# Performance work log

Hardware: AMD Instinct MI355X
Metric: run time of the kernel (lower is better)

## Reference

```python
import jax, jax.numpy as jnp
import numpy as np

B, TK, H = 32, 8192, 256

def setup_inputs() -> dict:
    key = jax.random.key(0)
    ks = jax.random.split(key, 10)
    s = 0.02
    return {
        "s_t_hat": jax.random.normal(ks[0], (B, 2 * H), dtype=jnp.float32),
        "encoder_outputs": jax.random.normal(ks[1], (B, TK, H), dtype=jnp.float32),
        "enc_padding_mask": jnp.ones((B, TK), dtype=jnp.float32),
        "coverage": jax.random.uniform(ks[2], (B, TK), dtype=jnp.float32),
        "attn_dist_node_to_token": jax.random.uniform(ks[3], (B, TK), dtype=jnp.float32),
        "We": jax.random.normal(ks[4], (H, H), dtype=jnp.float32) * s,   # encode_proj weight
        "Wd": jax.random.normal(ks[5], (H, 2 * H), dtype=jnp.float32) * s,  # decode_proj weight
        "bd": jax.random.normal(ks[6], (H,), dtype=jnp.float32) * s,     # decode_proj bias
        "wc": jax.random.normal(ks[7], (H,), dtype=jnp.float32) * s,     # W_c weight (Linear(1,H))
        "v": jax.random.normal(ks[8], (H,), dtype=jnp.float32) * s,      # v weight (Linear(H,1))
    }

def reference(s_t_hat, encoder_outputs, enc_padding_mask, coverage,
              attn_dist_node_to_token, We, Wd, bd, wc, v):
    # encoder projection: [b,t,h] @ We^T -> [b,t,h]
    enc_feat = jnp.einsum('bth,gh->btg', encoder_outputs, We)
    # decoder projection: [b,2h] @ Wd^T + bd -> [b,h]
    dec_fea = s_t_hat @ Wd.T + bd
    # coverage feature: outer product coverage[b,t] x wc[h]
    att_features = enc_feat + dec_fea[:, None, :] + coverage[..., None] * wc
    e = jnp.tanh(att_features)
    scores = jnp.einsum('bth,h->bt', e, v)  # [b, t_k]
    attn_ = jax.nn.softmax(scores, axis=1) * enc_padding_mask
    attn = attn_ / jnp.sum(attn_, axis=1, keepdims=True)
    c_t = jnp.einsum('bt,bth->bh', attn, encoder_outputs)  # context
    new_cov = jnp.clip(coverage + attn, 0.0, 1.0)
    return (c_t, attn, new_cov)
```

## Files before the change

### kernel.cpp

```cpp
#include <hip/hip_runtime.h>

#define B_  32
#define TK_ 8192
#define H_  256
#define MT  64

typedef __bf16 bf16_t;
typedef __bf16 bf16x4 __attribute__((ext_vector_type(4)));
typedef __bf16 bf16x8 __attribute__((ext_vector_type(8)));
typedef float  floatx4 __attribute__((ext_vector_type(4)));

__device__ __forceinline__ float tanh_fast(float x) {
    float e = __builtin_amdgcn_exp2f(x * 2.885390081777927f);
    return 1.0f - 2.0f * __builtin_amdgcn_rcpf(e + 1.0f);
}

__global__ void prep_kernel(const float* __restrict__ s_t_hat,
                            const float* __restrict__ We,
                            const float* __restrict__ Wd,
                            const float* __restrict__ bd,
                            bf16_t* __restrict__ We_bf,
                            float* __restrict__ dec_ws,
                            float* __restrict__ ctx_ws,
                            float* __restrict__ D_ws) {
    int tid = threadIdx.x, blk = blockIdx.x;
    int gid = blk * 256 + tid;
    We_bf[gid] = (bf16_t)We[gid];

    if (blk < 32) {
        ctx_ws[gid] = 0.f;
        if (gid < 32) D_ws[gid] = 0.f;
    }
    if (blk >= 32 && blk < 160) {
        int idx  = (blk - 32) * 256 + tid;
        int pair = idx >> 2, q = idx & 3;
        int b = pair >> 8, i = pair & 255;
        const float4* sp = (const float4*)(s_t_hat + b * 2 * H_ + q * 128);
        const float4* wp = (const float4*)(Wd + (size_t)i * 2 * H_ + q * 128);
        float sum = 0.f;
        #pragma unroll 8
        for (int ii = 0; ii < 32; ++ii) {
            float4 a = sp[ii], w = wp[ii];
            sum += a.x * w.x + a.y * w.y + a.z * w.z + a.w * w.w;
        }
        sum += __shfl_xor(sum, 1, 64);
        sum += __shfl_xor(sum, 2, 64);
        if (q == 0) dec_ws[pair] = sum + bd[i];
    }
}

__global__ __launch_bounds__(256, 3) void attn_main(
    const float* __restrict__ enc,
    const float* __restrict__ mask,
    const float* __restrict__ cov,
    const float* __restrict__ wc,
    const float* __restrict__ v,
    const bf16_t* __restrict__ We_bf,
    const float* __restrict__ dec_ws,
    float* __restrict__ ctx_ws,
    float* __restrict__ D_ws,
    float* __restrict__ attn_out) {

    __shared__ __align__(16) bf16_t As[MT * 264];
    __shared__ float dec_s[256], wc_s[256], v_s[256];
    __shared__ float cov_s[64], mask_s[64], wexp[64];
    __shared__ float sp[4][64];
    __shared__ float ctxp[4][256];

    const int tid  = threadIdx.x;
    const int b    = blockIdx.y;
    const int t0   = blockIdx.x * MT;
    const int lane = tid & 63, w = tid >> 6;
    const int l15  = lane & 15, l4 = lane >> 4;

    dec_s[tid] = dec_ws[b * 256 + tid];
    wc_s[tid]  = wc[tid];
    v_s[tid]   = v[tid];
    if (tid < 64)       cov_s[tid]       = cov[(size_t)b * TK_ + t0 + tid];
    else if (tid < 128) mask_s[tid - 64] = mask[(size_t)b * TK_ + t0 + tid - 64];

    const float* encb = enc + ((size_t)b * TK_ + t0) * H_;
    #pragma unroll
    for (int it = 0; it < 16; ++it) {
        int row = it * 4 + w;
        int h   = lane * 4;
        float4 f = *(const float4*)(encb + (size_t)row * H_ + h);
        bf16x4 p;
        p[0] = (bf16_t)f.x; p[1] = (bf16_t)f.y; p[2] = (bf16_t)f.z; p[3] = (bf16_t)f.w;
        *(bf16x4*)(&As[row * 264 + h]) = p;
    }
    __syncthreads();

    floatx4 acc[4][4];
    #pragma unroll
    for (int mi = 0; mi < 4; ++mi)
        #pragma unroll
        for (int ni = 0; ni < 4; ++ni)
            acc[mi][ni] = (floatx4){0.f, 0.f, 0.f, 0.f};

    const int wbase = w * 64;
    #pragma unroll
    for (int ks = 0; ks < 8; ++ks) {
        int k = ks * 32 + l4 * 8;
        bf16x8 a[4], bq[4];
        #pragma unroll
        for (int mi = 0; mi < 4; ++mi)
            a[mi] = *(const bf16x8*)(&As[(mi * 16 + l15) * 264 + k]);
        #pragma unroll
        for (int ni = 0; ni < 4; ++ni)
            bq[ni] = *(const bf16x8*)(We_bf + (size_t)(wbase + ni * 16 + l15) * 256 + k);
        #pragma unroll
        for (int mi = 0; mi < 4; ++mi)
            #pragma unroll
            for (int ni = 0; ni < 4; ++ni)
                acc[mi][ni] = __builtin_amdgcn_mfma_f32_16x16x32_bf16(
                    a[mi], bq[ni], acc[mi][ni], 0, 0, 0);
    }

    float decv[4], wcv[4], vv[4];
    #pragma unroll
    for (int ni = 0; ni < 4; ++ni) {
        int g = wbase + ni * 16 + l15;
        decv[ni] = dec_s[g]; wcv[ni] = wc_s[g]; vv[ni] = v_s[g];
    }
    #pragma unroll
    for (int mi = 0; mi < 4; ++mi) {
        #pragma unroll
        for (int r = 0; r < 4; ++r) {
            int t = mi * 16 + l4 * 4 + r;
            float cv = cov_s[t];
            float s = 0.f;
            #pragma unroll
            for (int ni = 0; ni < 4; ++ni) {
                float af = acc[mi][ni][r] + decv[ni] + cv * wcv[ni];
                s += tanh_fast(af) * vv[ni];
            }
            s += __shfl_xor(s, 1, 64);
            s += __shfl_xor(s, 2, 64);
            s += __shfl_xor(s, 4, 64);
            s += __shfl_xor(s, 8, 64);
            if (l15 == 0) sp[w][t] = s;
        }
    }
    __syncthreads();

    if (tid < 64) {
        int t = tid;
        float sc = sp[0][t] + sp[1][t] + sp[2][t] + sp[3][t];
        float wv = __builtin_amdgcn_exp2f(sc * 1.4426950408889634f) * mask_s[t];
        wexp[t] = wv;
        attn_out[(size_t)b * TK_ + t0 + t] = wv;
        float d = wv;
        d += __shfl_xor(d, 1, 64);  d += __shfl_xor(d, 2, 64);
        d += __shfl_xor(d, 4, 64);  d += __shfl_xor(d, 8, 64);
        d += __shfl_xor(d, 16, 64); d += __shfl_xor(d, 32, 64);
        if (tid == 0) atomicAdd(&D_ws[b], d);
    }
    __syncthreads();

    {
        int h0 = lane * 4;
        float c0 = 0, c1 = 0, c2 = 0, c3 = 0;
        #pragma unroll
        for (int tt = 0; tt < 16; ++tt) {
            int t = w * 16 + tt;
            float wv = wexp[t];
            bf16x4 q = *(const bf16x4*)(&As[t * 264 + h0]);
            c0 += wv * (float)q[0];
            c1 += wv * (float)q[1];
            c2 += wv * (float)q[2];
            c3 += wv * (float)q[3];
        }
        ctxp[w][h0 + 0] = c0; ctxp[w][h0 + 1] = c1;
        ctxp[w][h0 + 2] = c2; ctxp[w][h0 + 3] = c3;
    }
    __syncthreads();
    {
        float s = ctxp[0][tid] + ctxp[1][tid] + ctxp[2][tid] + ctxp[3][tid];
        atomicAdd(&ctx_ws[b * 256 + tid], s);
    }
}

__global__ void finalize_kernel(const float* __restrict__ cov,
                                const float* __restrict__ ctx_ws,
                                const float* __restrict__ D_ws,
                                float* __restrict__ out) {
    int b = blockIdx.y, chunk = blockIdx.x, tid = threadIdx.x;
    float invD = 1.0f / D_ws[b];
    int idx = chunk * 256 + tid;
    size_t gi = (size_t)b * TK_ + idx;
    float* attn = out + 8192;
    float* ncov = out + 8192 + (size_t)B_ * TK_;
    float a = attn[gi] * invD;
    attn[gi] = a;
    float nc = cov[gi] + a;
    ncov[gi] = fminf(fmaxf(nc, 0.f), 1.f);
    if (chunk == 0) out[b * 256 + tid] = ctx_ws[b * 256 + tid] * invD;
}

extern "C" void kernel_launch(void* const* d_in, const int* in_sizes, int n_in,
                              void* d_out, int out_size, void* d_ws, size_t ws_size,
                              hipStream_t stream) {
    const float* s_t_hat = (const float*)d_in[0];
    const float* enc     = (const float*)d_in[1];
    const float* mask    = (const float*)d_in[2];
    const float* cov     = (const float*)d_in[3];
    const float* We      = (const float*)d_in[5];
    const float* Wd      = (const float*)d_in[6];
    const float* bd      = (const float*)d_in[7];
    const float* wc      = (const float*)d_in[8];
    const float* v       = (const float*)d_in[9];
    float* out = (float*)d_out;

    char* ws = (char*)d_ws;
    bf16_t* We_bf = (bf16_t*)ws;
    float*  dec_ws = (float*)(ws + 131072);
    float*  ctx_ws = (float*)(ws + 131072 + 32768);
    float*  D_ws   = (float*)(ws + 131072 + 65536);

    prep_kernel<<<256, 256, 0, stream>>>(s_t_hat, We, Wd, bd, We_bf, dec_ws, ctx_ws, D_ws);
    attn_main<<<dim3(128, 32), 256, 0, stream>>>(enc, mask, cov, wc, v, We_bf,
                                                 dec_ws, ctx_ws, D_ws, out + 8192);
    finalize_kernel<<<dim3(32, 32), 256, 0, stream>>>(cov, ctx_ws, D_ws, out);
}
```

Measured before the change: 436.6 us.

## Replace global context atomics with per-block partials and prefetch weight fragments

Each block now writes its context partial sum to a per-block workspace slot instead of doing global float atomics, and finalize reduces the 128 partials per batch. The cross-wave reduction moves from a dedicated shared array to LDS atomics into the reused dec_s buffer, which frees shared memory. The launch bound goes from 3 to 4 blocks per CU, the encoder tile load is split into two batches of eight outstanding loads, and the B-operand weight fragments are register double-buffered across k-steps. The cost is more workspace traffic (about 4 MB of partials) and a serial 128-term reduction in finalize, plus register pressure from the prefetch under the tighter occupancy bound.

```diff
diff --git a/kernel.cpp b/kernel.cpp
--- a/kernel.cpp
+++ b/kernel.cpp
@@ -21,16 +21,13 @@
                             const float* __restrict__ bd,
                             bf16_t* __restrict__ We_bf,
                             float* __restrict__ dec_ws,
-                            float* __restrict__ ctx_ws,
                             float* __restrict__ D_ws) {
     int tid = threadIdx.x, blk = blockIdx.x;
     int gid = blk * 256 + tid;
     We_bf[gid] = (bf16_t)We[gid];
 
-    if (blk < 32) {
-        ctx_ws[gid] = 0.f;
-        if (gid < 32) D_ws[gid] = 0.f;
-    }
+    if (gid < 32) D_ws[gid] = 0.f;
+
     if (blk >= 32 && blk < 160) {
         int idx  = (blk - 32) * 256 + tid;
         int pair = idx >> 2, q = idx & 3;
@@ -49,7 +46,7 @@
     }
 }
 
-__global__ __launch_bounds__(256, 3) void attn_main(
+__global__ __launch_bounds__(256, 4) void attn_main(
     const float* __restrict__ enc,
     const float* __restrict__ mask,
     const float* __restrict__ cov,
@@ -57,7 +54,7 @@
     const float* __restrict__ v,
     const bf16_t* __restrict__ We_bf,
     const float* __restrict__ dec_ws,
-    float* __restrict__ ctx_ws,
+    float* __restrict__ ctx_part,
     float* __restrict__ D_ws,
     float* __restrict__ attn_out) {
 
@@ -65,7 +62,6 @@
     __shared__ float dec_s[256], wc_s[256], v_s[256];
     __shared__ float cov_s[64], mask_s[64], wexp[64];
     __shared__ float sp[4][64];
-    __shared__ float ctxp[4][256];
 
     const int tid  = threadIdx.x;
     const int b    = blockIdx.y;
@@ -80,14 +76,29 @@
     else if (tid < 128) mask_s[tid - 64] = mask[(size_t)b * TK_ + t0 + tid - 64];
 
     const float* encb = enc + ((size_t)b * TK_ + t0) * H_;
-    #pragma unroll
-    for (int it = 0; it < 16; ++it) {
-        int row = it * 4 + w;
-        int h   = lane * 4;
-        float4 f = *(const float4*)(encb + (size_t)row * H_ + h);
-        bf16x4 p;
-        p[0] = (bf16_t)f.x; p[1] = (bf16_t)f.y; p[2] = (bf16_t)f.z; p[3] = (bf16_t)f.w;
-        *(bf16x4*)(&As[row * 264 + h]) = p;
+    const int h4 = lane * 4;
+    {
+        float4 r[8];
+        #pragma unroll
+        for (int it = 0; it < 8; ++it)
+            r[it] = *(const float4*)(encb + (size_t)(it * 4 + w) * H_ + h4);
+        #pragma unroll
+        for (int it = 0; it < 8; ++it) {
+            bf16x4 p;
+            p[0] = (bf16_t)r[it].x; p[1] = (bf16_t)r[it].y;
+            p[2] = (bf16_t)r[it].z; p[3] = (bf16_t)r[it].w;
+            *(bf16x4*)(&As[(it * 4 + w) * 264 + h4]) = p;
+        }
+        #pragma unroll
+        for (int it = 0; it < 8; ++it)
+            r[it] = *(const float4*)(encb + (size_t)((it + 8) * 4 + w) * H_ + h4);
+        #pragma unroll
+        for (int it = 0; it < 8; ++it) {
+            bf16x4 p;
+            p[0] = (bf16_t)r[it].x; p[1] = (bf16_t)r[it].y;
+            p[2] = (bf16_t)r[it].z; p[3] = (bf16_t)r[it].w;
+            *(bf16x4*)(&As[((it + 8) * 4 + w) * 264 + h4]) = p;
+        }
     }
     __syncthreads();
 
@@ -99,22 +110,39 @@
             acc[mi][ni] = (floatx4){0.f, 0.f, 0.f, 0.f};
 
     const int wbase = w * 64;
+    const bf16_t* Bp = We_bf + (size_t)wbase * 256;
+    const int kf = l4 * 8;
+
+    bf16x8 bq[4];
+    #pragma unroll
+    for (int ni = 0; ni < 4; ++ni)
+        bq[ni] = *(const bf16x8*)(Bp + (size_t)(ni * 16 + l15) * 256 + kf);
+
     #pragma unroll
     for (int ks = 0; ks < 8; ++ks) {
-        int k = ks * 32 + l4 * 8;
-        bf16x8 a[4], bq[4];
+        bf16x8 bqn[4];
+        if (ks < 7) {
+            int kn = (ks + 1) * 32 + kf;
+            #pragma unroll
+            for (int ni = 0; ni < 4; ++ni)
+                bqn[ni] = *(const bf16x8*)(Bp + (size_t)(ni * 16 + l15) * 256 + kn);
+        }
+        int k = ks * 32 + kf;
+        bf16x8 a[4];
         #pragma unroll
         for (int mi = 0; mi < 4; ++mi)
             a[mi] = *(const bf16x8*)(&As[(mi * 16 + l15) * 264 + k]);
-        #pragma unroll
-        for (int ni = 0; ni < 4; ++ni)
-            bq[ni] = *(const bf16x8*)(We_bf + (size_t)(wbase + ni * 16 + l15) * 256 + k);
         #pragma unroll
         for (int mi = 0; mi < 4; ++mi)
             #pragma unroll
             for (int ni = 0; ni < 4; ++ni)
                 acc[mi][ni] = __builtin_amdgcn_mfma_f32_16x16x32_bf16(
                     a[mi], bq[ni], acc[mi][ni], 0, 0, 0);
+        if (ks < 7) {
+            #pragma unroll
+            for (int ni = 0; ni < 4; ++ni)
+                bq[ni] = bqn[ni];
+        }
     }
 
     float decv[4], wcv[4], vv[4];
@@ -156,6 +184,7 @@
         d += __shfl_xor(d, 16, 64); d += __shfl_xor(d, 32, 64);
         if (tid == 0) atomicAdd(&D_ws[b], d);
     }
+    dec_s[tid] = 0.f;
     __syncthreads();
 
     {
@@ -171,18 +200,17 @@
             c2 += wv * (float)q[2];
             c3 += wv * (float)q[3];
         }
-        ctxp[w][h0 + 0] = c0; ctxp[w][h0 + 1] = c1;
-        ctxp[w][h0 + 2] = c2; ctxp[w][h0 + 3] = c3;
-    }
-    __syncthreads();
-    {
-        float s = ctxp[0][tid] + ctxp[1][tid] + ctxp[2][tid] + ctxp[3][tid];
-        atomicAdd(&ctx_ws[b * 256 + tid], s);
-    }
+        atomicAdd(&dec_s[h0 + 0], c0);
+        atomicAdd(&dec_s[h0 + 1], c1);
+        atomicAdd(&dec_s[h0 + 2], c2);
+        atomicAdd(&dec_s[h0 + 3], c3);
+    }
+    __syncthreads();
+    ctx_part[((size_t)b * 128 + blockIdx.x) * 256 + tid] = dec_s[tid];
 }
 
 __global__ void finalize_kernel(const float* __restrict__ cov,
-                                const float* __restrict__ ctx_ws,
+                                const float* __restrict__ ctx_part,
                                 const float* __restrict__ D_ws,
                                 float* __restrict__ out) {
     int b = blockIdx.y, chunk = blockIdx.x, tid = threadIdx.x;
@@ -195,7 +223,18 @@
     attn[gi] = a;
     float nc = cov[gi] + a;
     ncov[gi] = fminf(fmaxf(nc, 0.f), 1.f);
-    if (chunk == 0) out[b * 256 + tid] = ctx_ws[b * 256 + tid] * invD;
+    if (chunk == 0) {
+        const float* p = ctx_part + (size_t)b * 128 * 256 + tid;
+        float s0 = 0, s1 = 0, s2 = 0, s3 = 0;
+        #pragma unroll 4
+        for (int j = 0; j < 128; j += 4) {
+            s0 += p[(j + 0) * 256];
+            s1 += p[(j + 1) * 256];
+            s2 += p[(j + 2) * 256];
+            s3 += p[(j + 3) * 256];
+        }
+        out[b * 256 + tid] = ((s0 + s1) + (s2 + s3)) * invD;
+    }
 }
 
 extern "C" void kernel_launch(void* const* d_in, const int* in_sizes, int n_in,
@@ -213,13 +252,13 @@
     float* out = (float*)d_out;
 
     char* ws = (char*)d_ws;
-    bf16_t* We_bf = (bf16_t*)ws;
+    bf16_t* We_bf  = (bf16_t*)ws;
     float*  dec_ws = (float*)(ws + 131072);
-    float*  ctx_ws = (float*)(ws + 131072 + 32768);
-    float*  D_ws   = (float*)(ws + 131072 + 65536);
-
-    prep_kernel<<<256, 256, 0, stream>>>(s_t_hat, We, Wd, bd, We_bf, dec_ws, ctx_ws, D_ws);
+    float*  D_ws   = (float*)(ws + 131072 + 32768);
+    float*  ctx_part = (float*)(ws + 131072 + 32768 + 256);
+
+    prep_kernel<<<256, 256, 0, stream>>>(s_t_hat, We, Wd, bd, We_bf, dec_ws, D_ws);
     attn_main<<<dim3(128, 32), 256, 0, stream>>>(enc, mask, cov, wc, v, We_bf,
-                                                 dec_ws, ctx_ws, D_ws, out + 8192);
-    finalize_kernel<<<dim3(32, 32), 256, 0, stream>>>(cov, ctx_ws, D_ws, out);
-}
+                                                 dec_ws, ctx_part, D_ws, out + 8192);
+    finalize_kernel<<<dim3(32, 32), 256, 0, stream>>>(cov, ctx_part, D_ws, out);
+}
```

After: 454.4 us. 1.04x slower.
